# Performance work log

Hardware: AMD Instinct MI355X
Metric: run time of the kernel (lower is better)

The kernel has to match this reference:

```python
import jax, jax.numpy as jnp
import numpy as np

NUM_NODES = 100_000
NUM_RELS = 64
DIM = 64
NUM_EDGES = 100_000


def setup_inputs() -> dict:
    key = jax.random.key(0)
    k_src, k_rel, k_dst, k_emb, k_w = jax.random.split(key, 5)
    src = jax.random.randint(k_src, (NUM_EDGES, 1), 0, NUM_NODES, dtype=jnp.int64 if jax.config.jax_enable_x64 else jnp.int32)
    rel = jax.random.randint(k_rel, (NUM_EDGES, 1), 0, NUM_RELS, dtype=src.dtype)
    dst = jax.random.randint(k_dst, (NUM_EDGES, 1), 0, NUM_NODES, dtype=src.dtype)
    triplets = jnp.concatenate([src, rel, dst], axis=1)  # [E, 3]
    node_emb = jax.random.normal(k_emb, (NUM_NODES, DIM), dtype=jnp.float32)
    # xavier_normal_ with gain=1.414: std = gain * sqrt(2 / (dim + dim))
    std = 1.414 * np.sqrt(2.0 / (DIM + DIM))
    W = jax.random.normal(k_w, (NUM_RELS, DIM, DIM), dtype=jnp.float32) * std
    return {"triplets": triplets, "node_emb": node_emb, "W": W}


def reference(triplets, node_emb, W):
    # score_e = src_emb_e^T @ W[rel_e] @ dst_emb_e  (per-edge bilinear form)
    src, rel, dst = triplets[:, 0], triplets[:, 1], triplets[:, 2]
    src_emb = node_emb[src]          # [E, d]
    dst_emb = node_emb[dst]          # [E, d]
    rel_emb = W[rel]                 # [E, d, d] gathered relation matrices
    scores = jnp.einsum('ed,edk,ek->e', src_emb, rel_emb, dst_emb)
    return scores
```

## Files before the change

kernel.cpp:

```cpp
#include <hip/hip_runtime.h>
#include <hip/hip_bf16.h>

#define NRELS 64
#define DIM 64
#define NSB 16
#define CSTRIDE 160
#define RSLOTS (NSB * CSTRIDE)
#define CHUNK 256
#define NCH (RSLOTS / CHUNK)
#define WLD 72

typedef __attribute__((ext_vector_type(8))) short short8;
typedef __attribute__((ext_vector_type(4))) float f32x4;

static __device__ __forceinline__ short bfc(float f) {
    union { __hip_bfloat16 h; short s; } u;
    u.h = __float2bfloat16(f);
    return u.s;
}
static __device__ __forceinline__ short8 pack8(float4 a, float4 b) {
    short8 o;
    o[0] = bfc(a.x); o[1] = bfc(a.y); o[2] = bfc(a.z); o[3] = bfc(a.w);
    o[4] = bfc(b.x); o[5] = bfc(b.y); o[6] = bfc(b.z); o[7] = bfc(b.w);
    return o;
}

__global__ __launch_bounds__(512)
void k_scatter(const int* __restrict__ trip, int E, int span,
               int* __restrict__ cnts, int4* __restrict__ bucket4) {
    __shared__ int lh[NRELS], lo[NRELS];
    const int t = threadIdx.x, b = blockIdx.x;
    if (t < NRELS) { lh[t] = 0; lo[t] = 0; }
    __syncthreads();
    const int elo = b * span, ehi = min(E, elo + span);
    for (int e = elo + t; e < ehi; e += 512)
        atomicAdd(&lh[trip[e * 3 + 1]], 1);
    __syncthreads();
    if (t < NRELS) cnts[b * NRELS + t] = min(lh[t], CSTRIDE);
    for (int e = elo + t; e < ehi; e += 512) {
        const int s = trip[e * 3], r = trip[e * 3 + 1], d = trip[e * 3 + 2];
        const int p = atomicAdd(&lo[r], 1);
        if (p < CSTRIDE)
            bucket4[r * RSLOTS + b * CSTRIDE + p] = make_int4(s, d, e, 0);
    }
}

__global__ __launch_bounds__(512)
void k_score(const float* __restrict__ emb, const float* __restrict__ W,
             const int* __restrict__ cnts, const int4* __restrict__ bucket4,
             float* __restrict__ out) {
    const int r = blockIdx.x, ch = blockIdx.y;
    __shared__ short Wl[DIM][WLD];
    __shared__ int cntL[NSB];
    const int t = threadIdx.x;
    if (t < NSB) cntL[t] = cnts[t * NRELS + r];
    {
        const float4* __restrict__ Wr = (const float4*)(W + (long)r * DIM * DIM);
        #pragma unroll
        for (int k = 0; k < 2; ++k) {
            const int j = t + k * 512;
            const float4 v = Wr[j];
            const int d = j >> 4, n0 = (j & 15) * 4;
            Wl[n0 + 0][d] = bfc(v.x);
            Wl[n0 + 1][d] = bfc(v.y);
            Wl[n0 + 2][d] = bfc(v.z);
            Wl[n0 + 3][d] = bfc(v.w);
        }
    }
    __syncthreads();

    const int lane = t & 63, wave = t >> 6;
    const int w0 = ch * CHUNK + wave * 32;
    const int col = lane & 15, kg = lane >> 4, kb = kg * 8;

    const int slot0 = w0 + col, slot1 = slot0 + 16;
    const int c0 = slot0 / CSTRIDE, c1 = slot1 / CSTRIDE;
    const bool v0 = (slot0 - c0 * CSTRIDE) < cntL[c0];
    const bool v1 = (slot1 - c1 * CSTRIDE) < cntL[c1];
    if (__ballot(v0 || v1) == 0ull) return;

    const int4 raw0 = bucket4[r * RSLOTS + slot0];
    const int4 raw1 = bucket4[r * RSLOTS + slot1];
    const int sI0 = v0 ? raw0.x : 0;
    const int sI1 = v1 ? raw1.x : 0;
    const int dv0 = v0 ? raw0.y : 0;
    const int dv1 = v1 ? raw1.y : 0;
    const int ev0 = v0 ? raw0.z : -1;
    const int ev1 = v1 ? raw1.z : -1;

    const float* __restrict__ s0 = emb + (long)sI0 * DIM;
    const float* __restrict__ s1 = emb + (long)sI1 * DIM;
    float4 f0 = *(const float4*)(s0 + kb),      f1 = *(const float4*)(s0 + kb + 4);
    float4 f2 = *(const float4*)(s0 + 32 + kb), f3 = *(const float4*)(s0 + 32 + kb + 4);
    const short8 a00 = pack8(f0, f1), a01 = pack8(f2, f3);
    f0 = *(const float4*)(s1 + kb);      f1 = *(const float4*)(s1 + kb + 4);
    f2 = *(const float4*)(s1 + 32 + kb); f3 = *(const float4*)(s1 + 32 + kb + 4);
    const short8 a10 = pack8(f0, f1), a11 = pack8(f2, f3);

    f32x4 acc0[4], acc1[4];
    #pragma unroll
    for (int q = 0; q < 4; ++q) {
        acc0[q] = (f32x4){0.f, 0.f, 0.f, 0.f};
        acc1[q] = (f32x4){0.f, 0.f, 0.f, 0.f};
    }
    #pragma unroll
    for (int q = 0; q < 4; ++q) {
        const short8 b0 = *(const short8*)&Wl[q * 16 + col][kb];
        const short8 b1 = *(const short8*)&Wl[q * 16 + col][32 + kb];
        acc0[q] = __builtin_amdgcn_mfma_f32_16x16x32_bf16(a00, b0, acc0[q], 0, 0, 0);
        acc0[q] = __builtin_amdgcn_mfma_f32_16x16x32_bf16(a01, b1, acc0[q], 0, 0, 0);
        acc1[q] = __builtin_amdgcn_mfma_f32_16x16x32_bf16(a10, b0, acc1[q], 0, 0, 0);
        acc1[q] = __builtin_amdgcn_mfma_f32_16x16x32_bf16(a11, b1, acc1[q], 0, 0, 0);
    }

    #pragma unroll
    for (int s2 = 0; s2 < 2; ++s2) {
        const f32x4* acc = s2 ? acc1 : acc0;
        const int dsrc = s2 ? dv1 : dv0;
        const int esrc = s2 ? ev1 : ev0;
        #pragma unroll
        for (int rr = 0; rr < 4; ++rr) {
            const int j = kg * 4 + rr;
            const int dIdx = __shfl(dsrc, j, 64);
            const int eIdx = __shfl(esrc, j, 64);
            const float* __restrict__ dr = emb + (long)dIdx * DIM;
            float p = acc[0][rr] * dr[col]
                    + acc[1][rr] * dr[16 + col]
                    + acc[2][rr] * dr[32 + col]
                    + acc[3][rr] * dr[48 + col];
            #pragma unroll
            for (int m = 1; m <= 8; m <<= 1) p += __shfl_xor(p, m, 64);
            if (col == 0 && eIdx >= 0) out[eIdx] = p;
        }
    }
}

extern "C" void kernel_launch(void* const* d_in, const int* in_sizes, int n_in,
                              void* d_out, int out_size, void* d_ws, size_t ws_size,
                              hipStream_t stream) {
    const int*   trip = (const int*)d_in[0];
    const float* emb  = (const float*)d_in[1];
    const float* W    = (const float*)d_in[2];
    float*       out  = (float*)d_out;

    const int E = in_sizes[0] / 3;
    const int span = (E + NSB - 1) / NSB;

    int4* bucket4 = (int4*)d_ws;
    int*  cnts    = (int*)(bucket4 + NRELS * RSLOTS);

    k_scatter<<<NSB, 512, 0, stream>>>(trip, E, span, cnts, bucket4);
    k_score  <<<dim3(NRELS, NCH), 512, 0, stream>>>(emb, W, cnts, bucket4, out);
}
```

Baseline: 25.99 us.

## Compact per-relation buckets via prefix sums and shrink score grid

The score kernel now computes a prefix sum of the per-sub-block counts for each relation and maps a dense logical index onto the padded bucket slots. Valid edges are packed contiguously, so waves no longer land on sparse padding, and blocks or waves past the total count exit early, before the W load when possible. The grid's chunk dimension is cut from 10 to 8, which covers 2048 edges per relation, more than the expected roughly 1563. This adds a small scan and a per-lane search over 16 prefixes, and edges beyond 2048 for a single relation would be dropped.

New measurement: 26.76 us. +3.0%, slower.

```diff
diff --git a/kernel.cpp b/kernel.cpp
--- a/kernel.cpp
+++ b/kernel.cpp
@@ -7,7 +7,7 @@
 #define CSTRIDE 160
 #define RSLOTS (NSB * CSTRIDE)
 #define CHUNK 256
-#define NCH (RSLOTS / CHUNK)
+#define NCH 8
 #define WLD 72
 
 typedef __attribute__((ext_vector_type(8))) short short8;
@@ -51,9 +51,24 @@
              float* __restrict__ out) {
     const int r = blockIdx.x, ch = blockIdx.y;
     __shared__ short Wl[DIM][WLD];
-    __shared__ int cntL[NSB];
+    __shared__ __align__(16) int pfxL[NSB + 4];
     const int t = threadIdx.x;
-    if (t < NSB) cntL[t] = cnts[t * NRELS + r];
+
+    if (t < 64) {
+        int v = (t < NSB) ? cnts[t * NRELS + r] : 0;
+        int pfx = v;
+        #pragma unroll
+        for (int d = 1; d < NSB; d <<= 1) {
+            const int up = __shfl_up(pfx, d, 64);
+            if (t >= d) pfx += up;
+        }
+        if (t < NSB) pfxL[t + 1] = pfx;
+        if (t == 0) pfxL[0] = 0;
+    }
+    __syncthreads();
+    const int total = pfxL[NSB];
+    if (ch * CHUNK >= total) return;
+
     {
         const float4* __restrict__ Wr = (const float4*)(W + (long)r * DIM * DIM);
         #pragma unroll
@@ -71,16 +86,36 @@
 
     const int lane = t & 63, wave = t >> 6;
     const int w0 = ch * CHUNK + wave * 32;
+    if (w0 >= total) return;
     const int col = lane & 15, kg = lane >> 4, kb = kg * 8;
 
-    const int slot0 = w0 + col, slot1 = slot0 + 16;
-    const int c0 = slot0 / CSTRIDE, c1 = slot1 / CSTRIDE;
-    const bool v0 = (slot0 - c0 * CSTRIDE) < cntL[c0];
-    const bool v1 = (slot1 - c1 * CSTRIDE) < cntL[c1];
-    if (__ballot(v0 || v1) == 0ull) return;
+    int pfx[NSB + 1];
+    {
+        const int4* __restrict__ p4 = (const int4*)pfxL;
+        #pragma unroll
+        for (int q = 0; q < 4; ++q) {
+            const int4 v = p4[q];
+            pfx[q * 4 + 0] = v.x; pfx[q * 4 + 1] = v.y;
+            pfx[q * 4 + 2] = v.z; pfx[q * 4 + 3] = v.w;
+        }
+        pfx[NSB] = total;
+    }
 
-    const int4 raw0 = bucket4[r * RSLOTS + slot0];
-    const int4 raw1 = bucket4[r * RSLOTS + slot1];
+    const int j0 = w0 + col, j1 = j0 + 16;
+    int c0 = 0, c1 = 0, base0 = 0, base1 = 0;
+    #pragma unroll
+    for (int b = 1; b < NSB; ++b) {
+        const bool g0 = (j0 >= pfx[b]);
+        const bool g1 = (j1 >= pfx[b]);
+        c0 += g0; base0 = g0 ? pfx[b] : base0;
+        c1 += g1; base1 = g1 ? pfx[b] : base1;
+    }
+    const bool v0 = j0 < total, v1 = j1 < total;
+    const int idx0 = v0 ? (r * RSLOTS + c0 * CSTRIDE + (j0 - base0)) : r * RSLOTS;
+    const int idx1 = v1 ? (r * RSLOTS + c1 * CSTRIDE + (j1 - base1)) : r * RSLOTS;
+
+    const int4 raw0 = bucket4[idx0];
+    const int4 raw1 = bucket4[idx1];
     const int sI0 = v0 ? raw0.x : 0;
     const int sI1 = v1 ? raw1.x : 0;
     const int dv0 = v0 ? raw0.y : 0;
@@ -120,9 +155,9 @@
         const int esrc = s2 ? ev1 : ev0;
         #pragma unroll
         for (int rr = 0; rr < 4; ++rr) {
-            const int j = kg * 4 + rr;
-            const int dIdx = __shfl(dsrc, j, 64);
-            const int eIdx = __shfl(esrc, j, 64);
+            const int jown = kg * 4 + rr;
+            const int dIdx = __shfl(dsrc, jown, 64);
+            const int eIdx = __shfl(esrc, jown, 64);
             const float* __restrict__ dr = emb + (long)dIdx * DIM;
             float p = acc[0][rr] * dr[col]
                     + acc[1][rr] * dr[16 + col]
```

## Transpose MFMA operands so each lane owns an edge; drop scatter histogram pass

Applied to the files above, without the earlier changes.

Swaps the A and B operands of the bf16 MFMA so the accumulator is laid out with edges along columns. Each lane then holds one edge's projected row and does its dst dot product with float4 loads and two cross-group shuffles, with no per-row index shuffles or 16-lane reductions. The scatter kernel also drops its separate histogram pass and writes the clamped counts from the slot atomics after the bucketing loop. This trades fewer shuffles and scalar loads for a different accumulator mapping that must match the MFMA output layout exactly.

Result: faster. 24.34 us (-6.3%).

```diff
diff --git a/kernel.cpp b/kernel.cpp
--- a/kernel.cpp
+++ b/kernel.cpp
@@ -28,21 +28,19 @@
 __global__ __launch_bounds__(512)
 void k_scatter(const int* __restrict__ trip, int E, int span,
                int* __restrict__ cnts, int4* __restrict__ bucket4) {
-    __shared__ int lh[NRELS], lo[NRELS];
+    __shared__ int lo[NRELS];
     const int t = threadIdx.x, b = blockIdx.x;
-    if (t < NRELS) { lh[t] = 0; lo[t] = 0; }
+    if (t < NRELS) lo[t] = 0;
     __syncthreads();
     const int elo = b * span, ehi = min(E, elo + span);
-    for (int e = elo + t; e < ehi; e += 512)
-        atomicAdd(&lh[trip[e * 3 + 1]], 1);
-    __syncthreads();
-    if (t < NRELS) cnts[b * NRELS + t] = min(lh[t], CSTRIDE);
     for (int e = elo + t; e < ehi; e += 512) {
         const int s = trip[e * 3], r = trip[e * 3 + 1], d = trip[e * 3 + 2];
         const int p = atomicAdd(&lo[r], 1);
         if (p < CSTRIDE)
             bucket4[r * RSLOTS + b * CSTRIDE + p] = make_int4(s, d, e, 0);
     }
+    __syncthreads();
+    if (t < NRELS) cnts[b * NRELS + t] = min(lo[t], CSTRIDE);
 }
 
 __global__ __launch_bounds__(512)
@@ -107,31 +105,41 @@
     for (int q = 0; q < 4; ++q) {
         const short8 b0 = *(const short8*)&Wl[q * 16 + col][kb];
         const short8 b1 = *(const short8*)&Wl[q * 16 + col][32 + kb];
-        acc0[q] = __builtin_amdgcn_mfma_f32_16x16x32_bf16(a00, b0, acc0[q], 0, 0, 0);
-        acc0[q] = __builtin_amdgcn_mfma_f32_16x16x32_bf16(a01, b1, acc0[q], 0, 0, 0);
-        acc1[q] = __builtin_amdgcn_mfma_f32_16x16x32_bf16(a10, b0, acc1[q], 0, 0, 0);
-        acc1[q] = __builtin_amdgcn_mfma_f32_16x16x32_bf16(a11, b1, acc1[q], 0, 0, 0);
+        acc0[q] = __builtin_amdgcn_mfma_f32_16x16x32_bf16(b0, a00, acc0[q], 0, 0, 0);
+        acc0[q] = __builtin_amdgcn_mfma_f32_16x16x32_bf16(b1, a01, acc0[q], 0, 0, 0);
+        acc1[q] = __builtin_amdgcn_mfma_f32_16x16x32_bf16(b0, a10, acc1[q], 0, 0, 0);
+        acc1[q] = __builtin_amdgcn_mfma_f32_16x16x32_bf16(b1, a11, acc1[q], 0, 0, 0);
     }
 
-    #pragma unroll
-    for (int s2 = 0; s2 < 2; ++s2) {
-        const f32x4* acc = s2 ? acc1 : acc0;
-        const int dsrc = s2 ? dv1 : dv0;
-        const int esrc = s2 ? ev1 : ev0;
+    {
+        const float* __restrict__ dr = emb + (long)dv0 * DIM;
+        float p = 0.f;
         #pragma unroll
-        for (int rr = 0; rr < 4; ++rr) {
-            const int j = kg * 4 + rr;
-            const int dIdx = __shfl(dsrc, j, 64);
-            const int eIdx = __shfl(esrc, j, 64);
-            const float* __restrict__ dr = emb + (long)dIdx * DIM;
-            float p = acc[0][rr] * dr[col]
-                    + acc[1][rr] * dr[16 + col]
-                    + acc[2][rr] * dr[32 + col]
-                    + acc[3][rr] * dr[48 + col];
-            #pragma unroll
-            for (int m = 1; m <= 8; m <<= 1) p += __shfl_xor(p, m, 64);
-            if (col == 0 && eIdx >= 0) out[eIdx] = p;
+        for (int q = 0; q < 4; ++q) {
+            const float4 dv = *(const float4*)(dr + q * 16 + kg * 4);
+            p = fmaf(acc0[q][0], dv.x, p);
+            p = fmaf(acc0[q][1], dv.y, p);
+            p = fmaf(acc0[q][2], dv.z, p);
+            p = fmaf(acc0[q][3], dv.w, p);
         }
+        p += __shfl_xor(p, 16, 64);
+        p += __shfl_xor(p, 32, 64);
+        if (kg == 0 && ev0 >= 0) out[ev0] = p;
+    }
+    {
+        const float* __restrict__ dr = emb + (long)dv1 * DIM;
+        float p = 0.f;
+        #pragma unroll
+        for (int q = 0; q < 4; ++q) {
+            const float4 dv = *(const float4*)(dr + q * 16 + kg * 4);
+            p = fmaf(acc1[q][0], dv.x, p);
+            p = fmaf(acc1[q][1], dv.y, p);
+            p = fmaf(acc1[q][2], dv.z, p);
+            p = fmaf(acc1[q][3], dv.w, p);
+        }
+        p += __shfl_xor(p, 16, 64);
+        p += __shfl_xor(p, 32, 64);
+        if (kg == 0 && ev1 >= 0) out[ev1] = p;
     }
 }
 
```
